# Performance work log

Hardware: AMD Instinct MI355X
Metric: run time of the kernel (lower is better)

Reference implementation:

```python
import jax, jax.numpy as jnp
import numpy as np

# ---- static configuration (matches init_kwargs) ----
N_QUBITS = 11
N_LAYERS = 2
N_HIDDEN = N_QUBITS // 2            # 5
N_VISIBLE = N_QUBITS - N_HIDDEN     # 6
N_PARAMS = N_LAYERS * (3 * N_HIDDEN + (N_HIDDEN - 1) + 3 * N_VISIBLE)  # 74
TWO_PI = 2.0 * np.pi

# Pauli building blocks (numpy constants, complex64)
I2 = np.eye(2, dtype=np.complex64)
X2 = np.array([[0, 1], [1, 0]], dtype=np.complex64)
K2 = np.array([[0, -1], [1, 0]], dtype=np.complex64)   # -i*Y
Z2 = np.array([[1, 0], [0, -1]], dtype=np.complex64)

# PauliZ sign table: wire 0 is the most-significant bit of the flattened state
_idx = np.arange(2 ** N_QUBITS)
SIGNS = np.stack([1.0 - 2.0 * ((_idx >> (N_QUBITS - 1 - q)) & 1)
                  for q in range(N_QUBITS)], 0).astype(np.float32)  # [n_qubits, 2^n]


def _rx(t):
    t = jnp.asarray(t, jnp.float32)
    c, s = jnp.cos(t / 2), jnp.sin(t / 2)
    return (c[..., None, None] * I2 - 1j * s[..., None, None] * X2).astype(jnp.complex64)


def _ry(t):
    t = jnp.asarray(t, jnp.float32)
    c, s = jnp.cos(t / 2), jnp.sin(t / 2)
    return (c[..., None, None] * I2 + s[..., None, None] * K2).astype(jnp.complex64)


def _rz(t):
    t = jnp.asarray(t, jnp.float32)
    c, s = jnp.cos(t / 2), jnp.sin(t / 2)
    return (c[..., None, None] * I2 - 1j * s[..., None, None] * Z2).astype(jnp.complex64)


def _apply_1q(state, gate, q):
    # state: (B,) + (2,)*N_QUBITS ; gate: [2,2] shared or [B,2,2] batched
    s = jnp.moveaxis(state, 1 + q, -1)
    if gate.ndim == 3:
        s = jnp.einsum('bij,b...j->b...i', gate, s)
    else:
        s = jnp.einsum('ij,...j->...i', gate, s)
    return jnp.moveaxis(s, -1, 1 + q)


def _apply_crx(state, theta, c, t):
    # controlled-RX(theta) with control wire c, target wire t (theta scalar)
    sc = jnp.moveaxis(state, [1 + c, 1 + t], [1, 2])
    g = _rx(theta)  # [2,2]
    s1 = jnp.einsum('ij,bj...->bi...', g, sc[:, 1])
    sc = jnp.stack([sc[:, 0], s1], axis=1)
    return jnp.moveaxis(sc, [1, 2], [1 + c, 1 + t])


def _embed_state(angles):
    # Angle embedding: RX(angle_q)|0> on each wire -> product state
    B = angles.shape[0]
    amp = _rx(angles)[..., :, 0]          # [B, n_qubits, 2] (first column = action on |0>)
    st = amp[:, 0]                        # [B, 2]
    for q in range(1, N_QUBITS):
        st = (st[:, :, None] * amp[:, q][:, None, :]).reshape(B, -1)
    return st.reshape((B,) + (2,) * N_QUBITS)


def _circuit(angles, params):
    st = _embed_state(angles)
    p = 0
    for _ in range(N_LAYERS):
        for i in range(N_HIDDEN):
            st = _apply_1q(st, _rx(params[p]), i)
            st = _apply_1q(st, _ry(params[p + 1]), i)
            st = _apply_1q(st, _rz(params[p + 2]), i)
            p += 3
        for i in range(N_HIDDEN - 1):
            st = _apply_crx(st, params[p], i, i + 1)
            p += 1
        for i in range(N_VISIBLE):
            w = N_HIDDEN + i
            st = _apply_1q(st, _rx(params[p]), w)
            st = _apply_1q(st, _ry(params[p + 1]), w)
            st = _apply_1q(st, _rz(params[p + 2]), w)
            p += 3
    probs = (st.real ** 2 + st.imag ** 2).reshape(st.shape[0], -1)  # [B, 2^n]
    return jnp.einsum('bi,qi->bq', probs, SIGNS)  # <Z_q> per qubit, [B, n_qubits]


def _preprocess(x_t):
    # mean-pool feature vector down to n_visible, then min-max scale to [0, 2pi]
    F = x_t.shape[-1]
    step = F // N_VISIBLE
    starts = np.arange(N_VISIBLE) * step
    win = x_t[:, starts[:, None] + np.arange(step)]   # [B, n_visible, step]
    pooled = win.mean(-1)
    mn = pooled.min(-1, keepdims=True)
    mx = pooled.max(-1, keepdims=True)
    return TWO_PI * (pooled - mn) / (mx - mn + 1e-8)


def setup_inputs() -> dict:
    key = jax.random.key(0)
    k1, k2 = jax.random.split(key)
    x = jax.random.normal(k1, (128, 48, 60), dtype=jnp.float32)
    hidden = jnp.zeros((128, N_HIDDEN), dtype=jnp.float32)
    params = jax.random.uniform(k2, (N_PARAMS,), dtype=jnp.float32,
                                minval=0.0, maxval=TWO_PI)
    return {"x": x, "hidden": hidden, "params": params}


def reference(x, hidden, params):
    def body(h, x_t):
        inp = _preprocess(x_t)                         # [B, n_visible]
        angles = jnp.concatenate([h, inp], axis=-1)    # [B, n_qubits]
        z = _circuit(angles, params)                   # [B, n_qubits]
        return z[:, :N_HIDDEN], z[:, N_HIDDEN:]

    xs = jnp.swapaxes(x, 0, 1)                         # [S, B, F]
    hidden_final, outs = jax.lax.scan(body, hidden, xs)
    outputs = jnp.swapaxes(outs, 0, 1)                 # [B, S, n_visible]
    return outputs, hidden_final
```

## Files before the change

### kernel.cpp

```cpp
#include <hip/hip_runtime.h>
#include <math.h>

#define TSTEPS 48
#define FEAT 60
#define BATCH 128
#define BLOCK 256
#define TWO_PI_F 6.2831853071795864769f


struct Cf { float r, i; };
__device__ __forceinline__ Cf cmul(Cf a, Cf b){ return {a.r*b.r - a.i*b.i, a.r*b.i + a.i*b.r}; }
__device__ __forceinline__ Cf cadd(Cf a, Cf b){ return {a.r+b.r, a.i+b.i}; }
__device__ __forceinline__ void mm2(const Cf A[4], const Cf B[4], Cf D[4]) {
  D[0] = cadd(cmul(A[0],B[0]), cmul(A[1],B[2]));
  D[1] = cadd(cmul(A[0],B[1]), cmul(A[1],B[3]));
  D[2] = cadd(cmul(A[2],B[0]), cmul(A[3],B[2]));
  D[3] = cadd(cmul(A[2],B[1]), cmul(A[3],B[3]));
}

__device__ __forceinline__ void fusedU(const float* p, Cf U[4]) {
  float cx = cosf(0.5f*p[0]), sxn = sinf(0.5f*p[0]);
  float cy = cosf(0.5f*p[1]), syn = sinf(0.5f*p[1]);
  float cz = cosf(0.5f*p[2]), szn = sinf(0.5f*p[2]);
  Cf RX[4] = {{cx,0.f},{0.f,-sxn},{0.f,-sxn},{cx,0.f}};
  Cf RY[4] = {{cy,0.f},{-syn,0.f},{syn,0.f},{cy,0.f}};
  Cf RZ[4] = {{cz,-szn},{0.f,0.f},{0.f,0.f},{cz,szn}};
  Cf M[4];
  mm2(RY, RX, M);
  mm2(RZ, M, U);
}

template<int CTRL>
__device__ __forceinline__ float dppf(float v) {
  return __int_as_float(__builtin_amdgcn_mov_dpp(__float_as_int(v), CTRL, 0xF, 0xF, true));
}

template<int M>
__device__ __forceinline__ float sx(float v) {
  if constexpr (M == 1)      return dppf<0xB1>(v);
  else if constexpr (M == 2) return dppf<0x4E>(v);
  else if constexpr (M == 3) return dppf<0x1B>(v);
  else if constexpr (M == 4) return dppf<0x141>(dppf<0x1B>(v));
  else                       return dppf<0x128>(v);
}

__device__ __forceinline__ float wave_sum(float v) {
  v += sx<1>(v);
  v += sx<2>(v);
  v += sx<4>(v);
  v += sx<8>(v);
  v += dppf<0x142>(v);
  v += dppf<0x143>(v);
  return __int_as_float(__builtin_amdgcn_readlane(__float_as_int(v), 63));
}

__device__ __forceinline__ float2 conjmul(float2 a, float2 b) {
  return make_float2(a.x*b.x + a.y*b.y, a.x*b.y - a.y*b.x);
}

__device__ __forceinline__ void contract_q(const float2* __restrict__ src,
                                           float2* __restrict__ dst,
                                           const float2* __restrict__ Pq,
                                           int NT, int D, int tid) {
  const int total = 3*NT*D*D;
  const int bs = 2*D;
  for (int tau = tid; tau < total; tau += BLOCK) {
    int K = tau % D;
    int rr = tau / D;
    int J = rr % D; rr /= D;
    int t = rr % NT;
    int s2 = rr / NT;
    const float2* Sb = src + t*(bs*bs);
    const float2* Pm = Pq + s2*4;
    float ax = 0.f, ay = 0.f;
    #pragma unroll
    for (int a = 0; a < 2; ++a)
      #pragma unroll
      for (int bb = 0; bb < 2; ++bb) {
        float2 g = Sb[(2*J+a)*bs + (2*K+bb)];
        float2 p = Pm[bb*2 + a];
        ax += g.x*p.x - g.y*p.y;
        ay += g.x*p.y + g.y*p.x;
      }
    dst[tau] = make_float2(ax, ay);
  }
}

__global__ __launch_bounds__(BLOCK)
void qrnn_kernel(const float* __restrict__ x, const float* __restrict__ hin,
                 const float* __restrict__ params, float* __restrict__ out) {
  __shared__ float2 G5[5*1024];
  __shared__ __align__(16) char uAV[16800];
  __shared__ float coefL[5*256];
  __shared__ float2 Pl[5*12];
  __shared__ float2 U2l[5*4];
  __shared__ float crxcl[8], crxsl[8];
  __shared__ float Wl[6*8];

  const int b   = blockIdx.x;
  const int tid = threadIdx.x;

  float2* Vp = (float2*)uAV;
  float2* A1 = (float2*)uAV;
  float2* A2 = (float2*)(uAV + 6144);
  float2* A3 = (float2*)(uAV + 10752);
  float2* A4 = (float2*)(uAV + 14208);

  if (tid < 5) {
    int q = tid;
    Cf U1[4]; fusedU(params + 3*q, U1);
    Cf T[4] = {U1[0], {-U1[1].r,-U1[1].i}, U1[2], {-U1[3].r,-U1[3].i}};
    Cf Ud[4] = {{U1[0].r,-U1[0].i},{U1[2].r,-U1[2].i},
                {U1[1].r,-U1[1].i},{U1[3].r,-U1[3].i}};
    Cf Zt[4]; mm2(T, Ud, Zt);
    Cf Ty[4] = {{-U1[1].i, U1[1].r}, {U1[0].i, -U1[0].r},
                {-U1[3].i, U1[3].r}, {U1[2].i, -U1[2].r}};
    Cf Yt[4]; mm2(Ty, Ud, Yt);
    float2* P = Pl + q*12;
    P[0] = make_float2(1.f,0.f); P[1] = make_float2(0.f,0.f);
    P[2] = make_float2(0.f,0.f); P[3] = make_float2(1.f,0.f);
    #pragma unroll
    for (int e = 0; e < 4; ++e) P[4+e] = make_float2(Zt[e].r, Zt[e].i);
    #pragma unroll
    for (int e = 0; e < 4; ++e) P[8+e] = make_float2(-Yt[e].r, -Yt[e].i);
  } else if (tid >= 8 && tid < 13) {
    int q = tid - 8;
    Cf U2[4]; fusedU(params + 37 + 3*q, U2);
    #pragma unroll
    for (int e = 0; e < 4; ++e) U2l[q*4+e] = make_float2(U2[e].r, U2[e].i);
  } else if (tid >= 16 && tid < 24) {
    int i = tid - 16;
    float th = (i < 4) ? params[15 + i] : params[52 + (i - 4)];
    crxcl[i] = cosf(0.5f*th); crxsl[i] = sinf(0.5f*th);
  } else if (tid >= 24 && tid < 30) {
    int k = tid - 24;
    Cf Ua[4], Ub[4], W[4];
    fusedU(params + 19 + 3*k, Ua);
    fusedU(params + 56 + 3*k, Ub);
    mm2(Ub, Ua, W);
    #pragma unroll
    for (int e = 0; e < 4; ++e) { Wl[k*8+2*e] = W[e].r; Wl[k*8+2*e+1] = W[e].i; }
  }
  __syncthreads();

  for (int e = tid; e < 1024; e += BLOCK)
    Vp[e] = make_float2(((e >> 5) == (e & 31)) ? 1.f : 0.f, 0.f);
  __syncthreads();

  #pragma unroll 1
  for (int g = 0; g < 4; ++g) {
    const int pt = 3 - g;
    const float hc = crxcl[g], hs = crxsl[g];
    for (int tau = tid; tau < 256; tau += BLOCK) {
      int col = tau & 31, pr = tau >> 5;
      int r0 = ((pr >> pt) << (pt+2)) | (1 << (pt+1)) | (pr & ((1 << pt) - 1));
      int r1 = r0 | (1 << pt);
      float2 a = Vp[r0*32+col], bb = Vp[r1*32+col];
      Vp[r0*32+col] = make_float2(hc*a.x + hs*bb.y, hc*a.y - hs*bb.x);
      Vp[r1*32+col] = make_float2(hs*a.y + hc*bb.x, -hs*a.x + hc*bb.y);
    }
    __syncthreads();
  }
  #pragma unroll 1
  for (int q = 0; q < 5; ++q) {
    const int p = 4 - q;
    float2 u0 = U2l[q*4+0], u1 = U2l[q*4+1], u2 = U2l[q*4+2], u3 = U2l[q*4+3];
    for (int tau = tid; tau < 512; tau += BLOCK) {
      int col = tau & 31, pr = tau >> 5;
      int r0 = ((pr >> p) << (p+1)) | (pr & ((1 << p) - 1));
      int r1 = r0 | (1 << p);
      float2 a = Vp[r0*32+col], bb = Vp[r1*32+col];
      Vp[r0*32+col] = make_float2(u0.x*a.x - u0.y*a.y + u1.x*bb.x - u1.y*bb.y,
                                  u0.x*a.y + u0.y*a.x + u1.x*bb.y + u1.y*bb.x);
      Vp[r1*32+col] = make_float2(u2.x*a.x - u2.y*a.y + u3.x*bb.x - u3.y*bb.y,
                                  u2.x*a.y + u2.y*a.x + u3.x*bb.y + u3.y*bb.x);
    }
    __syncthreads();
  }
  #pragma unroll 1
  for (int g = 0; g < 4; ++g) {
    const int pt = 3 - g;
    const float hc = crxcl[4+g], hs = crxsl[4+g];
    for (int tau = tid; tau < 256; tau += BLOCK) {
      int col = tau & 31, pr = tau >> 5;
      int r0 = ((pr >> pt) << (pt+2)) | (1 << (pt+1)) | (pr & ((1 << pt) - 1));
      int r1 = r0 | (1 << pt);
      float2 a = Vp[r0*32+col], bb = Vp[r1*32+col];
      Vp[r0*32+col] = make_float2(hc*a.x + hs*bb.y, hc*a.y - hs*bb.x);
      Vp[r1*32+col] = make_float2(hs*a.y + hc*bb.x, -hs*a.x + hc*bb.y);
    }
    __syncthreads();
  }

  {
    const int jt = tid >> 4, kt = tid & 15;
    float2 acc[5][2][2];
    #pragma unroll
    for (int m = 0; m < 5; ++m)
      #pragma unroll
      for (int a = 0; a < 2; ++a)
        #pragma unroll
        for (int c2 = 0; c2 < 2; ++c2) acc[m][a][c2] = make_float2(0.f, 0.f);
    #pragma unroll 4
    for (int i = 0; i < 32; ++i) {
      float2 vj0 = Vp[i*32 + 2*jt], vj1 = Vp[i*32 + 2*jt + 1];
      float2 vk0 = Vp[i*32 + 2*kt], vk1 = Vp[i*32 + 2*kt + 1];
      float2 p00 = conjmul(vj0, vk0), p01 = conjmul(vj0, vk1);
      float2 p10 = conjmul(vj1, vk0), p11 = conjmul(vj1, vk1);
      #pragma unroll
      for (int m = 0; m < 5; ++m) {
        float sg = ((i >> (4 - m)) & 1) ? -1.f : 1.f;
        acc[m][0][0].x = fmaf(sg, p00.x, acc[m][0][0].x);
        acc[m][0][0].y = fmaf(sg, p00.y, acc[m][0][0].y);
        acc[m][0][1].x = fmaf(sg, p01.x, acc[m][0][1].x);
        acc[m][0][1].y = fmaf(sg, p01.y, acc[m][0][1].y);
        acc[m][1][0].x = fmaf(sg, p10.x, acc[m][1][0].x);
        acc[m][1][0].y = fmaf(sg, p10.y, acc[m][1][0].y);
        acc[m][1][1].x = fmaf(sg, p11.x, acc[m][1][1].x);
        acc[m][1][1].y = fmaf(sg, p11.y, acc[m][1][1].y);
      }
    }
    #pragma unroll
    for (int m = 0; m < 5; ++m)
      #pragma unroll
      for (int a = 0; a < 2; ++a)
        #pragma unroll
        for (int c2 = 0; c2 < 2; ++c2)
          G5[m*1024 + (2*jt + a)*32 + (2*kt + c2)] = acc[m][a][c2];
  }
  __syncthreads();

  #pragma unroll 1
  for (int m = 0; m < 5; ++m) {
    contract_q(G5 + m*1024, A1, Pl + 4*12, 1, 16, tid);   __syncthreads();
    contract_q(A1,          A2, Pl + 3*12, 3,  8, tid);   __syncthreads();
    contract_q(A2,          A3, Pl + 2*12, 9,  4, tid);   __syncthreads();
    contract_q(A3,          A4, Pl + 1*12, 27, 2, tid);   __syncthreads();
    for (int tau = tid; tau < 256; tau += BLOCK) {
      float val = 0.f;
      if (tau < 243) {
        int t = tau % 81, s2 = tau / 81;
        const float2* Sb = A4 + t*4;
        const float2* Pm = Pl + 0*12 + s2*4;
        float ax = 0.f;
        #pragma unroll
        for (int a = 0; a < 2; ++a)
          #pragma unroll
          for (int bb = 0; bb < 2; ++bb) {
            float2 g = Sb[a*2 + bb];
            float2 p = Pm[bb*2 + a];
            ax += g.x*p.x - g.y*p.y;
          }
        val = ax * (1.f/32.f);
      }
      coefL[m*256 + tau] = val;
    }
    __syncthreads();
  }

  const int w = tid >> 6, lane = tid & 63;
  if (w == 0) {
    float sA[4][5], sB[4][5], sC[4][5], cf[5][4];
    #pragma unroll
    for (int j = 0; j < 4; ++j) {
      int n = j*64 + lane;
      int nn = (n < 243) ? n : 0;
      int d0 = nn/81; int rm = nn - d0*81;
      int d1 = rm/27; rm -= d1*27;
      int d2 = rm/9;  rm -= d2*9;
      int d3 = rm/3;  int d4 = rm - d3*3;
      int dq[5] = {d0, d1, d2, d3, d4};
      #pragma unroll
      for (int q = 0; q < 5; ++q) {
        sA[j][q] = (dq[q] == 0) ? 1.f : 0.f;
        sB[j][q] = (dq[q] == 1) ? 1.f : 0.f;
        sC[j][q] = (dq[q] == 2) ? 1.f : 0.f;
      }
      #pragma unroll
      for (int m = 0; m < 5; ++m) cf[m][j] = coefL[m*256 + n];
    }
    const float* hp = hin + b*5;
    float h0 = hp[0], h1 = hp[1], h2 = hp[2], h3 = hp[3], h4 = hp[4];
    #pragma unroll 1
    for (int t = 0; t < TSTEPS; ++t) {
      float cq0 = __cosf(h0), sq0 = __sinf(h0);
      float cq1 = __cosf(h1), sq1 = __sinf(h1);
      float cq2 = __cosf(h2), sq2 = __sinf(h2);
      float cq3 = __cosf(h3), sq3 = __sinf(h3);
      float cq4 = __cosf(h4), sq4 = __sinf(h4);
      float cq[5] = {cq0, cq1, cq2, cq3, cq4};
      float sq[5] = {sq0, sq1, sq2, sq3, sq4};
      float mono[4];
      #pragma unroll
      for (int j = 0; j < 4; ++j) {
        float f0 = fmaf(sB[j][0], cq[0], fmaf(sC[j][0], sq[0], sA[j][0]));
        float f1 = fmaf(sB[j][1], cq[1], fmaf(sC[j][1], sq[1], sA[j][1]));
        float f2 = fmaf(sB[j][2], cq[2], fmaf(sC[j][2], sq[2], sA[j][2]));
        float f3 = fmaf(sB[j][3], cq[3], fmaf(sC[j][3], sq[3], sA[j][3]));
        float f4 = fmaf(sB[j][4], cq[4], fmaf(sC[j][4], sq[4], sA[j][4]));
        mono[j] = ((f0*f1)*(f2*f3))*f4;
      }
      float hn[5];
      #pragma unroll
      for (int m = 0; m < 5; ++m) {
        float p01 = fmaf(cf[m][1], mono[1], cf[m][0]*mono[0]);
        float p23 = fmaf(cf[m][3], mono[3], cf[m][2]*mono[2]);
        hn[m] = wave_sum(p01 + p23);
      }
      h0 = hn[0]; h1 = hn[1]; h2 = hn[2]; h3 = hn[3]; h4 = hn[4];
    }
    if (lane < 5) {
      float hv = (lane==0) ? h0 : (lane==1) ? h1 : (lane==2) ? h2
               : (lane==3) ? h3 : h4;
      out[BATCH*TSTEPS*6 + b*5 + lane] = hv;
    }
  } else if (w == 1 && lane < TSTEPS) {
    const float* xp = x + (size_t)b*(TSTEPS*FEAT) + lane*FEAT;
    const float4* xp4 = (const float4*)xp;
    float4 vv[15];
    #pragma unroll
    for (int i2 = 0; i2 < 15; ++i2) vv[i2] = xp4[i2];
    float el[60];
    #pragma unroll
    for (int i2 = 0; i2 < 15; ++i2) {
      el[4*i2+0] = vv[i2].x; el[4*i2+1] = vv[i2].y;
      el[4*i2+2] = vv[i2].z; el[4*i2+3] = vv[i2].w;
    }
    float pooled[6];
    #pragma unroll
    for (int k = 0; k < 6; ++k) {
      float s = 0.f;
      #pragma unroll
      for (int f = 0; f < 10; ++f) s += el[k*10 + f];
      pooled[k] = s * 0.1f;
    }
    float mn = pooled[0], mx = pooled[0];
    #pragma unroll
    for (int v2 = 1; v2 < 6; ++v2) {
      mn = fminf(mn, pooled[v2]); mx = fmaxf(mx, pooled[v2]);
    }
    float* op = out + (size_t)b*(TSTEPS*6) + lane*6;
    #pragma unroll
    for (int k = 0; k < 6; ++k) {
      float W0r = Wl[k*8+0], W0i = Wl[k*8+1], W1r = Wl[k*8+2], W1i = Wl[k*8+3];
      float W2r = Wl[k*8+4], W2i = Wl[k*8+5], W3r = Wl[k*8+6], W3i = Wl[k*8+7];
      float ang = TWO_PI_F * (pooled[k] - mn) / (mx - mn + 1e-8f);
      float ch = __cosf(0.5f*ang), sh = __sinf(0.5f*ang);
      float v0r = W0r*ch + W1i*sh, v0i = W0i*ch - W1r*sh;
      float v1r = W2r*ch + W3i*sh, v1i = W2i*ch - W3r*sh;
      op[k] = (v0r*v0r + v0i*v0i) - (v1r*v1r + v1i*v1i);
    }
  }
}

extern "C" void kernel_launch(void* const* d_in, const int* in_sizes, int n_in,
                              void* d_out, int out_size, void* d_ws, size_t ws_size,
                              hipStream_t stream) {
  const float* x      = (const float*)d_in[0];
  const float* hidden = (const float*)d_in[1];
  const float* params = (const float*)d_in[2];
  float* out          = (float*)d_out;
  qrnn_kernel<<<dim3(BATCH), dim3(BLOCK), 0, stream>>>(x, hidden, params, out);
}
```

Before: 94.86 us.

## Apply hidden-qubit gates in registers and batch contraction stages across observables

The 13 separate shared-memory gate passes over the 32x32 hidden operator, each followed by a barrier, are replaced by a single register pass. Each thread holds four amplitudes and applies gates with DPP lane swaps and in-register butterflies. The Gram accumulation now sums a total plus per-bit partial sums instead of five signed accumulators, and folds the first Pauli contraction into the same pass. The remaining contraction stages run once for all five observables instead of looping per observable, which cuts the barrier count, at the cost of larger ping-pong shared buffers and more register pressure.

```diff
diff --git a/kernel.cpp b/kernel.cpp
--- a/kernel.cpp
+++ b/kernel.cpp
@@ -44,6 +44,9 @@
   else                       return dppf<0x128>(v);
 }
 
+template<int M>
+__device__ __forceinline__ Cf sxc(Cf v){ return { sx<M>(v.r), sx<M>(v.i) }; }
+
 __device__ __forceinline__ float wave_sum(float v) {
   v += sx<1>(v);
   v += sx<2>(v);
@@ -58,26 +61,76 @@
   return make_float2(a.x*b.x + a.y*b.y, a.x*b.y - a.y*b.x);
 }
 
-__device__ __forceinline__ void contract_q(const float2* __restrict__ src,
-                                           float2* __restrict__ dst,
-                                           const float2* __restrict__ Pq,
-                                           int NT, int D, int tid) {
-  const int total = 3*NT*D*D;
-  const int bs = 2*D;
+template<int M>
+__device__ __forceinline__ void lane_u(Cf A[4], const Cf U[4], int hi) {
+  Cf ca = hi ? U[3] : U[0];
+  Cf cb = hi ? U[2] : U[1];
+  #pragma unroll
+  for (int r = 0; r < 4; ++r) {
+    Cf o = sxc<M>(A[r]);
+    A[r] = cadd(cmul(ca, A[r]), cmul(cb, o));
+  }
+}
+template<int M>
+__device__ __forceinline__ void lane_crx(Cf A[4], float c, float s, int cv) {
+  float cc = cv ? c : 1.f, ss = cv ? s : 0.f;
+  #pragma unroll
+  for (int r = 0; r < 4; ++r) {
+    Cf o = sxc<M>(A[r]);
+    A[r] = { cc*A[r].r + ss*o.i, cc*A[r].i - ss*o.r };
+  }
+}
+__device__ __forceinline__ void reg_u_b1(Cf A[4], const Cf U[4]) {
+  #pragma unroll
+  for (int k = 0; k < 2; ++k) {
+    Cf a0 = A[k], a1 = A[k+2];
+    A[k]   = cadd(cmul(U[0], a0), cmul(U[1], a1));
+    A[k+2] = cadd(cmul(U[2], a0), cmul(U[3], a1));
+  }
+}
+__device__ __forceinline__ void reg_u_b0(Cf A[4], const Cf U[4]) {
+  #pragma unroll
+  for (int k = 0; k < 4; k += 2) {
+    Cf a0 = A[k], a1 = A[k+1];
+    A[k]   = cadd(cmul(U[0], a0), cmul(U[1], a1));
+    A[k+1] = cadd(cmul(U[2], a0), cmul(U[3], a1));
+  }
+}
+__device__ __forceinline__ void reg_crx_b1(Cf A[4], float c, float s, int cv) {
+  float cc = cv ? c : 1.f, ss = cv ? s : 0.f;
+  #pragma unroll
+  for (int k = 0; k < 2; ++k) {
+    Cf a0 = A[k], a1 = A[k+2];
+    A[k]   = { cc*a0.r + ss*a1.i, cc*a0.i - ss*a1.r };
+    A[k+2] = { ss*a0.i + cc*a1.r, -ss*a0.r + cc*a1.i };
+  }
+}
+__device__ __forceinline__ void reg_crx_b0c1(Cf A[4], float c, float s) {
+  Cf a0 = A[2], a1 = A[3];
+  A[2] = { c*a0.r + s*a1.i, c*a0.i - s*a1.r };
+  A[3] = { s*a0.i + c*a1.r, -s*a0.r + c*a1.i };
+}
+
+template<int NTs, int D>
+__device__ __forceinline__ void stageK(const float2* __restrict__ src,
+                                       float2* __restrict__ dst,
+                                       const float2* __restrict__ Pq, int tid) {
+  const int total = 5*3*NTs*D*D;
   for (int tau = tid; tau < total; tau += BLOCK) {
     int K = tau % D;
-    int rr = tau / D;
-    int J = rr % D; rr /= D;
-    int t = rr % NT;
-    int s2 = rr / NT;
-    const float2* Sb = src + t*(bs*bs);
-    const float2* Pm = Pq + s2*4;
+    int J = (tau / D) % D;
+    int rest = tau / (D*D);
+    int t = rest % NTs;
+    int s = (rest / NTs) % 3;
+    int m = rest / (3*NTs);
+    const float2* Sb = src + (m*NTs + t)*(4*D*D);
+    const float2* Pm = Pq + s*4;
     float ax = 0.f, ay = 0.f;
     #pragma unroll
     for (int a = 0; a < 2; ++a)
       #pragma unroll
       for (int bb = 0; bb < 2; ++bb) {
-        float2 g = Sb[(2*J+a)*bs + (2*K+bb)];
+        float2 g = Sb[(2*J+a)*(2*D) + (2*K+bb)];
         float2 p = Pm[bb*2 + a];
         ax += g.x*p.x - g.y*p.y;
         ay += g.x*p.y + g.y*p.x;
@@ -89,8 +142,8 @@
 __global__ __launch_bounds__(BLOCK)
 void qrnn_kernel(const float* __restrict__ x, const float* __restrict__ hin,
                  const float* __restrict__ params, float* __restrict__ out) {
-  __shared__ float2 G5[5*1024];
-  __shared__ __align__(16) char uAV[16800];
+  __shared__ __align__(16) char bufA[30720];
+  __shared__ __align__(16) char bufB[23040];
   __shared__ float coefL[5*256];
   __shared__ float2 Pl[5*12];
   __shared__ float2 U2l[5*4];
@@ -100,11 +153,12 @@
   const int b   = blockIdx.x;
   const int tid = threadIdx.x;
 
-  float2* Vp = (float2*)uAV;
-  float2* A1 = (float2*)uAV;
-  float2* A2 = (float2*)(uAV + 6144);
-  float2* A3 = (float2*)(uAV + 10752);
-  float2* A4 = (float2*)(uAV + 14208);
+  float2* Vp  = (float2*)bufB;
+  float4* Vp4 = (float4*)bufB;
+  float2* A1  = (float2*)bufA;
+  float2* A2  = (float2*)bufB;
+  float2* A3  = (float2*)bufA;
+  float2* A4  = (float2*)bufB;
 
   if (tid < 5) {
     int q = tid;
@@ -143,120 +197,129 @@
   }
   __syncthreads();
 
-  for (int e = tid; e < 1024; e += BLOCK)
-    Vp[e] = make_float2(((e >> 5) == (e & 31)) ? 1.f : 0.f, 0.f);
+  {
+    const int quad = tid & 7, col = tid >> 3;
+    const int vb2 = quad & 1, vb3 = (quad >> 1) & 1, vb4 = quad >> 2;
+    Cf A[4];
+    #pragma unroll
+    for (int r = 0; r < 4; ++r)
+      A[r] = { ((quad<<2)|r) == col ? 1.f : 0.f, 0.f };
+    Cf U2g[5][4];
+    #pragma unroll
+    for (int q = 0; q < 5; ++q)
+      #pragma unroll
+      for (int e = 0; e < 4; ++e)
+        U2g[q][e] = { U2l[q*4+e].x, U2l[q*4+e].y };
+    float c_[8], s_[8];
+    #pragma unroll
+    for (int g = 0; g < 8; ++g) { c_[g] = crxcl[g]; s_[g] = crxsl[g]; }
+    lane_crx<2>(A, c_[0], s_[0], vb4);
+    lane_crx<1>(A, c_[1], s_[1], vb3);
+    reg_crx_b1 (A, c_[2], s_[2], vb2);
+    reg_crx_b0c1(A, c_[3], s_[3]);
+    lane_u<4>(A, U2g[0], vb4);
+    lane_u<2>(A, U2g[1], vb3);
+    lane_u<1>(A, U2g[2], vb2);
+    reg_u_b1 (A, U2g[3]);
+    reg_u_b0 (A, U2g[4]);
+    lane_crx<2>(A, c_[4], s_[4], vb4);
+    lane_crx<1>(A, c_[5], s_[5], vb3);
+    reg_crx_b1 (A, c_[6], s_[6], vb2);
+    reg_crx_b0c1(A, c_[7], s_[7]);
+    #pragma unroll
+    for (int r = 0; r < 4; ++r)
+      Vp[((quad<<2)|r)*32 + col] = make_float2(A[r].r, A[r].i);
+  }
   __syncthreads();
-
-  #pragma unroll 1
-  for (int g = 0; g < 4; ++g) {
-    const int pt = 3 - g;
-    const float hc = crxcl[g], hs = crxsl[g];
-    for (int tau = tid; tau < 256; tau += BLOCK) {
-      int col = tau & 31, pr = tau >> 5;
-      int r0 = ((pr >> pt) << (pt+2)) | (1 << (pt+1)) | (pr & ((1 << pt) - 1));
-      int r1 = r0 | (1 << pt);
-      float2 a = Vp[r0*32+col], bb = Vp[r1*32+col];
-      Vp[r0*32+col] = make_float2(hc*a.x + hs*bb.y, hc*a.y - hs*bb.x);
-      Vp[r1*32+col] = make_float2(hs*a.y + hc*bb.x, -hs*a.x + hc*bb.y);
-    }
-    __syncthreads();
-  }
-  #pragma unroll 1
-  for (int q = 0; q < 5; ++q) {
-    const int p = 4 - q;
-    float2 u0 = U2l[q*4+0], u1 = U2l[q*4+1], u2 = U2l[q*4+2], u3 = U2l[q*4+3];
-    for (int tau = tid; tau < 512; tau += BLOCK) {
-      int col = tau & 31, pr = tau >> 5;
-      int r0 = ((pr >> p) << (p+1)) | (pr & ((1 << p) - 1));
-      int r1 = r0 | (1 << p);
-      float2 a = Vp[r0*32+col], bb = Vp[r1*32+col];
-      Vp[r0*32+col] = make_float2(u0.x*a.x - u0.y*a.y + u1.x*bb.x - u1.y*bb.y,
-                                  u0.x*a.y + u0.y*a.x + u1.x*bb.y + u1.y*bb.x);
-      Vp[r1*32+col] = make_float2(u2.x*a.x - u2.y*a.y + u3.x*bb.x - u3.y*bb.y,
-                                  u2.x*a.y + u2.y*a.x + u3.x*bb.y + u3.y*bb.x);
-    }
-    __syncthreads();
-  }
-  #pragma unroll 1
-  for (int g = 0; g < 4; ++g) {
-    const int pt = 3 - g;
-    const float hc = crxcl[4+g], hs = crxsl[4+g];
-    for (int tau = tid; tau < 256; tau += BLOCK) {
-      int col = tau & 31, pr = tau >> 5;
-      int r0 = ((pr >> pt) << (pt+2)) | (1 << (pt+1)) | (pr & ((1 << pt) - 1));
-      int r1 = r0 | (1 << pt);
-      float2 a = Vp[r0*32+col], bb = Vp[r1*32+col];
-      Vp[r0*32+col] = make_float2(hc*a.x + hs*bb.y, hc*a.y - hs*bb.x);
-      Vp[r1*32+col] = make_float2(hs*a.y + hc*bb.x, -hs*a.x + hc*bb.y);
-    }
-    __syncthreads();
-  }
 
   {
     const int jt = tid >> 4, kt = tid & 15;
-    float2 acc[5][2][2];
-    #pragma unroll
-    for (int m = 0; m < 5; ++m)
+    float2 T[2][2], Bm[5][2][2];
+    #pragma unroll
+    for (int a = 0; a < 2; ++a)
+      #pragma unroll
+      for (int c2 = 0; c2 < 2; ++c2) {
+        T[a][c2] = make_float2(0.f, 0.f);
+        #pragma unroll
+        for (int m = 0; m < 5; ++m) Bm[m][a][c2] = make_float2(0.f, 0.f);
+      }
+    #pragma unroll
+    for (int i = 0; i < 32; ++i) {
+      float4 vj = Vp4[i*16 + jt], vk = Vp4[i*16 + kt];
+      float2 vj0{vj.x,vj.y}, vj1{vj.z,vj.w}, vk0{vk.x,vk.y}, vk1{vk.z,vk.w};
+      float2 p[2][2] = {{conjmul(vj0,vk0), conjmul(vj0,vk1)},
+                        {conjmul(vj1,vk0), conjmul(vj1,vk1)}};
       #pragma unroll
       for (int a = 0; a < 2; ++a)
         #pragma unroll
-        for (int c2 = 0; c2 < 2; ++c2) acc[m][a][c2] = make_float2(0.f, 0.f);
-    #pragma unroll 4
-    for (int i = 0; i < 32; ++i) {
-      float2 vj0 = Vp[i*32 + 2*jt], vj1 = Vp[i*32 + 2*jt + 1];
-      float2 vk0 = Vp[i*32 + 2*kt], vk1 = Vp[i*32 + 2*kt + 1];
-      float2 p00 = conjmul(vj0, vk0), p01 = conjmul(vj0, vk1);
-      float2 p10 = conjmul(vj1, vk0), p11 = conjmul(vj1, vk1);
-      #pragma unroll
-      for (int m = 0; m < 5; ++m) {
-        float sg = ((i >> (4 - m)) & 1) ? -1.f : 1.f;
-        acc[m][0][0].x = fmaf(sg, p00.x, acc[m][0][0].x);
-        acc[m][0][0].y = fmaf(sg, p00.y, acc[m][0][0].y);
-        acc[m][0][1].x = fmaf(sg, p01.x, acc[m][0][1].x);
-        acc[m][0][1].y = fmaf(sg, p01.y, acc[m][0][1].y);
-        acc[m][1][0].x = fmaf(sg, p10.x, acc[m][1][0].x);
-        acc[m][1][0].y = fmaf(sg, p10.y, acc[m][1][0].y);
-        acc[m][1][1].x = fmaf(sg, p11.x, acc[m][1][1].x);
-        acc[m][1][1].y = fmaf(sg, p11.y, acc[m][1][1].y);
-      }
-    }
-    #pragma unroll
-    for (int m = 0; m < 5; ++m)
+        for (int c2 = 0; c2 < 2; ++c2) {
+          T[a][c2].x += p[a][c2].x; T[a][c2].y += p[a][c2].y;
+        }
+      #pragma unroll
+      for (int m = 0; m < 5; ++m)
+        if (i & (16 >> m)) {
+          #pragma unroll
+          for (int a = 0; a < 2; ++a)
+            #pragma unroll
+            for (int c2 = 0; c2 < 2; ++c2) {
+              Bm[m][a][c2].x += p[a][c2].x; Bm[m][a][c2].y += p[a][c2].y;
+            }
+        }
+    }
+    float2 P4[12];
+    #pragma unroll
+    for (int e = 0; e < 12; ++e) P4[e] = Pl[4*12 + e];
+    #pragma unroll
+    for (int m = 0; m < 5; ++m) {
+      float2 G[2][2];
       #pragma unroll
       for (int a = 0; a < 2; ++a)
         #pragma unroll
         for (int c2 = 0; c2 < 2; ++c2)
-          G5[m*1024 + (2*jt + a)*32 + (2*kt + c2)] = acc[m][a][c2];
-  }
-  __syncthreads();
-
-  #pragma unroll 1
-  for (int m = 0; m < 5; ++m) {
-    contract_q(G5 + m*1024, A1, Pl + 4*12, 1, 16, tid);   __syncthreads();
-    contract_q(A1,          A2, Pl + 3*12, 3,  8, tid);   __syncthreads();
-    contract_q(A2,          A3, Pl + 2*12, 9,  4, tid);   __syncthreads();
-    contract_q(A3,          A4, Pl + 1*12, 27, 2, tid);   __syncthreads();
-    for (int tau = tid; tau < 256; tau += BLOCK) {
-      float val = 0.f;
-      if (tau < 243) {
-        int t = tau % 81, s2 = tau / 81;
-        const float2* Sb = A4 + t*4;
-        const float2* Pm = Pl + 0*12 + s2*4;
-        float ax = 0.f;
+          G[a][c2] = make_float2(T[a][c2].x - 2.f*Bm[m][a][c2].x,
+                                 T[a][c2].y - 2.f*Bm[m][a][c2].y);
+      #pragma unroll
+      for (int s = 0; s < 3; ++s) {
+        float ax = 0.f, ay = 0.f;
         #pragma unroll
         for (int a = 0; a < 2; ++a)
           #pragma unroll
           for (int bb = 0; bb < 2; ++bb) {
-            float2 g = Sb[a*2 + bb];
-            float2 p = Pm[bb*2 + a];
+            float2 g = G[a][bb];
+            float2 p = P4[s*4 + bb*2 + a];
             ax += g.x*p.x - g.y*p.y;
+            ay += g.x*p.y + g.y*p.x;
           }
-        val = ax * (1.f/32.f);
-      }
-      coefL[m*256 + tau] = val;
-    }
-    __syncthreads();
-  }
+        A1[(m*3 + s)*256 + (jt<<4) + kt] = make_float2(ax, ay);
+      }
+    }
+  }
+  __syncthreads();
+
+  stageK<3, 8>(A1, A2, Pl + 3*12, tid);  __syncthreads();
+  stageK<9, 4>(A2, A3, Pl + 2*12, tid);  __syncthreads();
+  stageK<27,2>(A3, A4, Pl + 1*12, tid);  __syncthreads();
+  for (int tau = tid; tau < 5*256; tau += BLOCK) {
+    int n = tau & 255, m = tau >> 8;
+    float val = 0.f;
+    if (n < 243) {
+      int t = n % 81, s = n / 81;
+      const float2* Sb = A4 + (m*81 + t)*4;
+      const float2* Pm = Pl + s*4;
+      float ax = 0.f;
+      #pragma unroll
+      for (int a = 0; a < 2; ++a)
+        #pragma unroll
+        for (int bb = 0; bb < 2; ++bb) {
+          float2 g = Sb[a*2 + bb];
+          float2 p = Pm[bb*2 + a];
+          ax += g.x*p.x - g.y*p.y;
+        }
+      val = ax * (1.f/32.f);
+    }
+    coefL[tau] = val;
+  }
+  __syncthreads();
 
   const int w = tid >> 6, lane = tid & 63;
   if (w == 0) {
@@ -283,13 +346,8 @@
     float h0 = hp[0], h1 = hp[1], h2 = hp[2], h3 = hp[3], h4 = hp[4];
     #pragma unroll 1
     for (int t = 0; t < TSTEPS; ++t) {
-      float cq0 = __cosf(h0), sq0 = __sinf(h0);
-      float cq1 = __cosf(h1), sq1 = __sinf(h1);
-      float cq2 = __cosf(h2), sq2 = __sinf(h2);
-      float cq3 = __cosf(h3), sq3 = __sinf(h3);
-      float cq4 = __cosf(h4), sq4 = __sinf(h4);
-      float cq[5] = {cq0, cq1, cq2, cq3, cq4};
-      float sq[5] = {sq0, sq1, sq2, sq3, sq4};
+      float cq[5] = {__cosf(h0), __cosf(h1), __cosf(h2), __cosf(h3), __cosf(h4)};
+      float sq[5] = {__sinf(h0), __sinf(h1), __sinf(h2), __sinf(h3), __sinf(h4)};
       float mono[4];
       #pragma unroll
       for (int j = 0; j < 4; ++j) {
```

After: 89.17 us. 1.06x faster.
